# Kernel optimization log

Hardware: AMD Instinct MI355X
Metric: run time of the kernel (lower is better)

Reference implementation:

```python
import jax, jax.numpy as jnp
import numpy as np

FS = 16            # fixStride
LAST_RATIO = 0.5
TAUA, TAUB = 10.0, 0.1
TOT_EPOCHS = 100
EPS = 1e-20
SEED = 777


def _safe_norm(diff):
    # ||diff||_2 with subgradient 0 at 0 (matches torch.norm backward at 0)
    sq = jnp.sum(diff * diff, axis=-1)
    d = jnp.sqrt(jnp.where(sq > 0, sq, 1.0))
    return jnp.where(sq > 0, d, 0.0)


def _forward(x, w_score, b_score, att_params, num_graphs, epoch):
    BN, C = x.shape
    B = int(num_graphs)
    N = BN // B
    RES = N - FS + 1                       # rows per graph (unfold1d)
    MAXP = int(np.ceil(N * LAST_RATIO))    # max_pivot_count = ceil(N*last_ratio/init_ratio)

    # --- TopKPool scorer (init_ratio==1.0): permute nodes per graph by desc score
    scores = (x @ w_score + b_score) / jnp.sqrt(jnp.sum(w_score ** 2))
    perm = jnp.argsort(-scores.reshape(B, N), axis=-1, stable=True)      # [B,N]
    xg = jnp.take_along_axis(x.reshape(B, N, C), perm[..., None], axis=1)

    # --- sliding-window edges: row r -> dests r..r+FS-1, src node r
    dst = jnp.arange(RES)[:, None] + jnp.arange(FS)[None, :]             # [RES,FS]
    x_src = xg[:, :RES, :]                                               # [B,RES,C]
    x_dst = xg[:, dst, :]                                                # [B,RES,FS,C]

    # getSM_ei + scatter_softmax over rows: att = [x_s, x_d] @ att_params
    a1, a2 = att_params[:C], att_params[C:]
    sm = jax.nn.softmax((xg @ a1)[:, :RES, None] + (xg @ a2)[:, dst], axis=-1)  # [B,RES,FS]

    # getDM_ei (sigma=1): gaussian-kernel edge distances
    gk = jnp.exp(-_safe_norm(x_src[:, :, None, :] - x_dst) / 2.0) - EPS  # [B,RES,FS]

    # scatterSort: stable descending sort of gk per row
    order = jnp.argsort(-gk, axis=-1, stable=True)
    gk_sort = jnp.take_along_axis(gk, order, axis=-1)
    sm_sort = jnp.take_along_axis(sm, order, axis=-1)

    # per-rank column logits: scatter-sum of sorted attention over rows of each graph
    logits = jnp.broadcast_to(sm_sort.sum(axis=1)[:, None, :], (B, RES, FS))
    logits = logits.at[:, :, 0].set(-jnp.inf)            # mask rank-0 (self edge)

    # gumbel-softmax with annealed temperature
    tau0 = TAUA * (TAUB / TAUA) ** (float(epoch) / TOT_EPOCHS)
    g = jax.random.gumbel(jax.random.key(SEED), (B, RES, FS), jnp.float32)
    gmb = jax.nn.softmax((g + logits) / tau0, axis=-1)

    # per-row threshold and shifted distances (unsorted layout)
    ths = jnp.sum(gk_sort * gmb, axis=-1, keepdims=True)
    shifted = jax.nn.relu(gk - ths)                      # [B,RES,FS]

    # scatter_min over positions 1..FS-1 (position 0 excluded via index redirect)
    delta = (jnp.argmin(shifted[:, :, 1:], axis=-1) + 1).astype(jnp.int32)  # [B,RES]

    # innerLoopStar: follow skip pointers from row 0, up to MAXP pivots
    def chain(delta_g):
        def step(ptr, _):
            valid = ptr < RES
            piv = jnp.where(valid, ptr, -1)
            nxt = jnp.where(valid, ptr + delta_g[jnp.clip(ptr, 0, RES - 1)], jnp.int32(RES))
            return nxt, piv
        _, pivs = jax.lax.scan(step, jnp.int32(0), None, length=MAXP)
        return pivs

    pivots = jax.vmap(chain)(delta)                      # [B,MAXP], -1 padded
    mask = pivots >= 0
    pooled = jnp.take_along_axis(xg, jnp.clip(pivots, 0, N - 1)[..., None], axis=1)
    pooled = pooled * mask[..., None]                    # [B,MAXP,C]
    return pooled, shifted, pivots


def setup_inputs() -> dict:
    key = jax.random.key(0)
    k0, k1, k2, k3 = jax.random.split(key, 4)
    B, N, C = 128, 512, 64
    return {
        "x": jax.random.normal(k0, (B * N, C), jnp.float32),
        "w_score": jax.random.normal(k1, (C,), jnp.float32),
        "b_score": jax.random.normal(k2, (), jnp.float32),
        "att_params": jax.random.normal(k3, (2 * C,), jnp.float32),
        "num_graphs": B,
        "epoch": 10,
    }


def reference(x, w_score, b_score, att_params, num_graphs, epoch):
    return _forward(x, w_score, b_score, att_params, num_graphs, epoch)
```

## Files before the change

kernel.cpp:

```cpp
#include <hip/hip_runtime.h>
#include <math.h>

#define BB 128
#define NN 512
#define CC 64
#define FS 16
#define RES 497
#define MAXP 256
#define BN (BB*NN)
#define GT (BB*RES*FS)
#define WPB 16
#define NCH 32
#define ROWS (WPB+FS-1)
#define PITCH 66
#define TWPB 128
#define TCH 4

__device__ __forceinline__ unsigned rotl32(unsigned x, int d){ return (x<<d)|(x>>(32-d)); }

__device__ __forceinline__ void threefry777(unsigned x0, unsigned x1, unsigned &o0, unsigned &o1){
  const unsigned ks0 = 0u, ks1 = 777u;
  const unsigned ks2 = 0x1BD11BDAu ^ ks0 ^ ks1;
  x0 += ks0; x1 += ks1;
  x0+=x1; x1=rotl32(x1,13); x1^=x0;
  x0+=x1; x1=rotl32(x1,15); x1^=x0;
  x0+=x1; x1=rotl32(x1,26); x1^=x0;
  x0+=x1; x1=rotl32(x1, 6); x1^=x0;
  x0+=ks1; x1+=ks2+1u;
  x0+=x1; x1=rotl32(x1,17); x1^=x0;
  x0+=x1; x1=rotl32(x1,29); x1^=x0;
  x0+=x1; x1=rotl32(x1,16); x1^=x0;
  x0+=x1; x1=rotl32(x1,24); x1^=x0;
  x0+=ks2; x1+=ks0+2u;
  x0+=x1; x1=rotl32(x1,13); x1^=x0;
  x0+=x1; x1=rotl32(x1,15); x1^=x0;
  x0+=x1; x1=rotl32(x1,26); x1^=x0;
  x0+=x1; x1=rotl32(x1, 6); x1^=x0;
  x0+=ks0; x1+=ks1+3u;
  x0+=x1; x1=rotl32(x1,17); x1^=x0;
  x0+=x1; x1=rotl32(x1,29); x1^=x0;
  x0+=x1; x1=rotl32(x1,16); x1^=x0;
  x0+=x1; x1=rotl32(x1,24); x1^=x0;
  x0+=ks1; x1+=ks2+4u;
  x0+=x1; x1=rotl32(x1,13); x1^=x0;
  x0+=x1; x1=rotl32(x1,15); x1^=x0;
  x0+=x1; x1=rotl32(x1,26); x1^=x0;
  x0+=x1; x1=rotl32(x1, 6); x1^=x0;
  x0+=ks2; x1+=ks0+5u;
  o0 = x0; o1 = x1;
}

__device__ __forceinline__ float gumbel_at_f32(unsigned p){
  unsigned o0, o1;
  threefry777(0u, p, o0, o1);
  unsigned bits = o0 ^ o1;
  float fl = __uint_as_float((bits >> 9) | 0x3f800000u) - 1.0f;
  float u  = fmaxf(1.17549435e-38f, fl);
  return -logf(-logf(u));
}

__device__ __forceinline__ double wave_push_f64(double v, int dstLane){
  int lo = __double2loint(v), hi = __double2hiint(v);
  int plo = __builtin_amdgcn_ds_permute(dstLane<<2, lo);
  int phi = __builtin_amdgcn_ds_permute(dstLane<<2, hi);
  return __hiloint2double(phi, plo);
}

__global__ __launch_bounds__(NN) void k_scoresort(const float* __restrict__ x,
    const float* __restrict__ w, const float* __restrict__ bsc,
    const float* __restrict__ att, double* __restrict__ s1s,
    double* __restrict__ s2s, int* __restrict__ perm){
  int b = blockIdx.x, t = threadIdx.x;
  __shared__ double ss[NN];
  __shared__ int    si[NN];
  __shared__ double l1[NN], l2[NN];

  double wn=0.0, dw=0.0, d1=0.0, d2=0.0;
  #pragma unroll
  for (int c=0;c<CC;c++){ double wv=(double)w[c]; wn += wv*wv; }
  const float4* xr = (const float4*)(x + (size_t)(b*NN+t)*CC);
  #pragma unroll
  for (int q=0;q<CC/4;q++){
    float4 v = xr[q];
    double xv;
    xv=(double)v.x; dw+=xv*(double)w[4*q+0]; d1+=xv*(double)att[4*q+0]; d2+=xv*(double)att[CC+4*q+0];
    xv=(double)v.y; dw+=xv*(double)w[4*q+1]; d1+=xv*(double)att[4*q+1]; d2+=xv*(double)att[CC+4*q+1];
    xv=(double)v.z; dw+=xv*(double)w[4*q+2]; d1+=xv*(double)att[4*q+2]; d2+=xv*(double)att[CC+4*q+2];
    xv=(double)v.w; dw+=xv*(double)w[4*q+3]; d1+=xv*(double)att[4*q+3]; d2+=xv*(double)att[CC+4*q+3];
  }
  double s = (dw + (double)bsc[0]) / sqrt(wn);
  int idx = t;
  l1[t] = d1;
  l2[t] = d2;

  for (int k = 2; k <= NN; k <<= 1){
    bool up = ((t & k) == 0);
    for (int j = k >> 1; j >= 64; j >>= 1){
      ss[t] = s; si[t] = idx;
      __syncthreads();
      double os = ss[t ^ j]; int oi = si[t ^ j];
      bool first = ((t & j) == 0);
      bool cmp = (s > os) || (s == os && idx < oi);
      bool keep = (cmp == (first == up));
      if (!keep){ s = os; idx = oi; }
      __syncthreads();
    }
    #pragma unroll
    for (int j = 32; j > 0; j >>= 1){
      if (j <= (k >> 1)){
        double os = __shfl_xor(s, j, 64);
        int    oi = __shfl_xor(idx, j, 64);
        bool first = ((t & j) == 0);
        bool cmp = (s > os) || (s == os && idx < oi);
        bool keep = (cmp == (first == up));
        if (!keep){ s = os; idx = oi; }
      }
    }
  }
  __syncthreads();
  perm[b*NN + t] = idx;
  s1s[b*NN + t] = l1[idx];
  s2s[b*NN + t] = l2[idx];
}

__global__ __launch_bounds__(256) void k_passA(const float* __restrict__ x,
    const int* __restrict__ perm, const double* __restrict__ s1s,
    const double* __restrict__ s2s, double* __restrict__ gkd,
    unsigned char* __restrict__ rank8, double* __restrict__ partial){
  int b = blockIdx.y, ch = blockIdx.x, tid = threadIdx.x;
  int i0 = ch*WPB;
  int nwin  = min(WPB, RES - i0);
  int nrows = min(ROWS, NN - i0);
  __shared__ float  xs[ROWS*PITCH];
  __shared__ int    pg[ROWS];
  __shared__ double wred[4][FS];

  if (tid < nrows) pg[tid] = perm[b*NN + i0 + tid];
  __syncthreads();
  for (int u = tid; u < nrows*16; u += 256){
    int r = u >> 4, seg = u & 15;
    float4 v = ((const float4*)(x + (size_t)(b*NN + pg[r])*CC))[seg];
    float2* dst = (float2*)&xs[r*PITCH + seg*4];
    dst[0] = make_float2(v.x, v.y);
    dst[1] = make_float2(v.z, v.w);
  }
  __syncthreads();

  int w = tid >> 4, j = tid & 15;
  int lane = tid & 63, gbase = lane & 48, wv = tid >> 6;
  bool act = (w < nwin);
  int i = i0 + w;

  double sq = 0.0;
  const float* rs = &xs[w*PITCH];
  const float* rd = &xs[(w+j)*PITCH];
  #pragma unroll
  for (int c2=0;c2<CC/2;c2++){
    float2 a  = *(const float2*)&rs[2*c2];
    float2 bb = *(const float2*)&rd[2*c2];
    double d0 = (double)a.x - (double)bb.x;
    double d1v= (double)a.y - (double)bb.y;
    sq += d0*d0;
    sq += d1v*d1v;
  }
  double d   = (sq > 0.0) ? sqrt(sq) : 0.0;
  double gkv = exp(-d*0.5) - 1e-20;

  int drow = min(i + j, NN-1);
  double smt = s1s[b*NN + i] + s2s[b*NN + drow];
  double m = smt;
  #pragma unroll
  for (int off=8; off; off>>=1) m = fmax(m, __shfl_xor(m, off, 16));
  double em = exp(smt - m);
  double ssum = em;
  #pragma unroll
  for (int off=8; off; off>>=1) ssum += __shfl_xor(ssum, off, 16);
  double smn = em / ssum;

  int rank = 0;
  #pragma unroll
  for (int k=0;k<16;k++){
    double gkk = __shfl(gkv, gbase + k, 64);
    rank += ((gkk > gkv) || (gkk == gkv && k < j)) ? 1 : 0;
  }

  if (act){
    size_t base = ((size_t)b*RES + i)*FS;
    gkd[base + j]   = gkv;
    rank8[base + j] = (unsigned char)rank;
  }

  double contrib = act ? smn : 0.0;
  double srt = wave_push_f64(contrib, gbase + rank);
  srt += __shfl_xor(srt, 16, 64);
  srt += __shfl_xor(srt, 32, 64);
  if (lane < FS) wred[wv][lane] = srt;
  __syncthreads();
  if (tid < FS){
    partial[((size_t)b*NCH + ch)*FS + tid] =
        wred[0][tid] + wred[1][tid] + wred[2][tid] + wred[3][tid];
  }
}

__global__ __launch_bounds__(TWPB) void k_tail(const double* __restrict__ gkd,
    const unsigned char* __restrict__ rank8, const double* __restrict__ partial,
    const int* __restrict__ epoch_p, float* __restrict__ shifted_out,
    int* __restrict__ delta){
  int b = blockIdx.y, tid = threadIdx.x;
  int w0 = blockIdx.x*TWPB;
  int nw = min(TWPB, RES - w0);
  __shared__ double pl[NCH*FS];
  __shared__ double Ks[FS];
  __shared__ double gkL[TWPB*17];
  __shared__ double eL[TWPB*17];
  __shared__ uint4  rkL[TWPB];

  for (int u = tid; u < NCH*FS; u += TWPB) pl[u] = partial[(size_t)b*NCH*FS + u];
  {
    const double2* gsrc = (const double2*)(gkd + ((size_t)b*RES + w0)*FS);
    for (int u = tid; u < nw*8; u += TWPB){
      double2 v = gsrc[u];
      int row = u >> 3, col = (u & 7) << 1;
      gkL[row*17 + col]     = v.x;
      gkL[row*17 + col + 1] = v.y;
    }
  }
  if (tid < nw) rkL[tid] = ((const uint4*)rank8)[(size_t)b*RES + w0 + tid];
  __syncthreads();
  if (tid < FS){
    double a = 0.0;
    #pragma unroll
    for (int ch=0; ch<NCH; ch++) a += pl[ch*FS + tid];
    double tauB = 10.0 * exp(-4.605170185988091 * ((double)epoch_p[0] / 100.0));
    Ks[tid] = (tid == 0) ? 0.0 : exp(a / tauB);
  }
  __syncthreads();

  if (tid >= nw) return;
  int win = w0 + tid;
  size_t base = ((size_t)b*RES + win)*FS;
  double tau = 10.0 * exp(-4.605170185988091 * ((double)epoch_p[0] / 100.0));
  int gb = tid*17;

  eL[gb] = 0.0;
  double ssum = 0.0;
  for (int s=1;s<FS;s++){
    float g = gumbel_at_f32((unsigned)(base + (unsigned)s));
    double E = exp((double)g / tau) * Ks[s];
    eL[gb + s] = E;
    ssum += E;
  }

  uint4 rw = rkL[tid];
  unsigned rr[4] = { rw.x, rw.y, rw.z, rw.w };
  double ths = 0.0;
  #pragma unroll
  for (int j=0;j<FS;j++){
    int rk = (int)((rr[j>>2] >> ((j&3)*8)) & 15u);
    ths += gkL[gb + j] * (eL[gb + rk] / ssum);
  }

  double bv = 0.0; int bj = 1;
  #pragma unroll
  for (int q=0;q<4;q++){
    float4 sv;
    float* svp = (float*)&sv;
    #pragma unroll
    for (int r=0;r<4;r++){
      int j = q*4 + r;
      double shv = fmax(gkL[gb + j] - ths, 0.0);
      svp[r] = (float)shv;
      if (j == 1){ bv = shv; bj = 1; }
      else if (j > 1 && shv < bv){ bv = shv; bj = j; }
    }
    ((float4*)(shifted_out + base))[q] = sv;
  }
  delta[b*RES + win] = bj;
}

__global__ __launch_bounds__(256) void k_chainpool(const int* __restrict__ delta,
    const int* __restrict__ perm, const float* __restrict__ x,
    float* __restrict__ piv_out, float* __restrict__ pooled){
  int b = blockIdx.x, tid = threadIdx.x;
  __shared__ int tbl[8][512];
  __shared__ int pivS[MAXP];

  for (int i = tid; i < 512; i += 256){
    int v;
    if (i < RES){ v = i + delta[b*RES + i]; if (v > RES) v = RES; }
    else v = RES;
    tbl[0][i] = v;
  }
  __syncthreads();
  #pragma unroll
  for (int k=1;k<8;k++){
    int v0 = tbl[k-1][tid];
    int v1 = tbl[k-1][tid+256];
    tbl[k][tid]     = tbl[k-1][v0];
    tbl[k][tid+256] = tbl[k-1][v1];
    __syncthreads();
  }
  {
    int p = 0;
    #pragma unroll
    for (int k=0;k<8;k++) if ((tid>>k)&1) p = tbl[k][p];
    int piv = (p < RES) ? p : -1;
    pivS[tid] = piv;
    piv_out[b*MAXP + tid] = (float)piv;
  }
  __syncthreads();

  for (int u = tid; u < MAXP*16; u += 256){
    int bp = u >> 4, seg = u & 15;
    int piv = pivS[bp];
    float4 v = make_float4(0.f,0.f,0.f,0.f);
    if (piv >= 0){
      int src = perm[b*NN + piv];
      v = ((const float4*)(x + (size_t)(b*NN + src)*CC))[seg];
    }
    ((float4*)pooled)[(size_t)(b*MAXP + bp)*16 + seg] = v;
  }
}

extern "C" void kernel_launch(void* const* d_in, const int* in_sizes, int n_in,
                              void* d_out, int out_size, void* d_ws, size_t ws_size,
                              hipStream_t stream) {
  (void)in_sizes; (void)n_in; (void)out_size; (void)ws_size;
  const float* x    = (const float*)d_in[0];
  const float* w    = (const float*)d_in[1];
  const float* bsc  = (const float*)d_in[2];
  const float* att  = (const float*)d_in[3];
  const int*   epch = (const int*)d_in[5];

  double* s1s     = (double*)d_ws;
  double* s2s     = s1s + BN;
  double* gkd     = s2s + BN;
  double* partial = gkd + GT;
  int*    perm    = (int*)(partial + (size_t)BB*NCH*FS);
  int*    delta   = perm + BN;
  unsigned char* rank8 = (unsigned char*)(delta + BB*RES);

  float* out_pooled  = (float*)d_out;
  float* out_shifted = out_pooled + BB*MAXP*CC;
  float* out_piv     = out_shifted + (size_t)BB*RES*FS;

  k_scoresort<<<BB, NN, 0, stream>>>(x, w, bsc, att, s1s, s2s, perm);
  k_passA    <<<dim3(NCH, BB), 256, 0, stream>>>(x, perm, s1s, s2s, gkd, rank8, partial);
  k_tail     <<<dim3(TCH, BB), TWPB, 0, stream>>>(gkd, rank8, partial, epch, out_shifted, delta);
  k_chainpool<<<BB, 256, 0, stream>>>(delta, perm, x, out_piv, out_pooled);
}
```

Measured before the change: 70.18 us.

## Split each k_tail window across four lanes with shuffle reductions

The tail kernel now gives each sliding window to a group of four threads instead of one. Each lane computes four of the gumbel exponentials, loads four gk values and ranks directly from global memory, and writes one float4 of output. Partial sums, the threshold and the argmin are combined with wave shuffles. This raises parallelism (8x128 blocks of 256 threads) and shortens the serial per-thread gumbel and exp chains. In exchange it adds shuffle and synchronisation overhead and drops the shared-memory staging of gk.

```diff
diff --git a/kernel.cpp b/kernel.cpp
--- a/kernel.cpp
+++ b/kernel.cpp
@@ -13,8 +13,8 @@
 #define NCH 32
 #define ROWS (WPB+FS-1)
 #define PITCH 66
-#define TWPB 128
-#define TCH 4
+#define TW4 64
+#define TCH4 8
 
 __device__ __forceinline__ unsigned rotl32(unsigned x, int d){ return (x<<d)|(x>>(32-d)); }
 
@@ -202,80 +202,84 @@
   }
 }
 
-__global__ __launch_bounds__(TWPB) void k_tail(const double* __restrict__ gkd,
+__global__ __launch_bounds__(256) void k_tail(const double* __restrict__ gkd,
     const unsigned char* __restrict__ rank8, const double* __restrict__ partial,
     const int* __restrict__ epoch_p, float* __restrict__ shifted_out,
     int* __restrict__ delta){
   int b = blockIdx.y, tid = threadIdx.x;
-  int w0 = blockIdx.x*TWPB;
-  int nw = min(TWPB, RES - w0);
+  int grp = tid >> 2;
+  int L   = tid & 3;
+  int win = blockIdx.x*TW4 + grp;
   __shared__ double pl[NCH*FS];
   __shared__ double Ks[FS];
-  __shared__ double gkL[TWPB*17];
-  __shared__ double eL[TWPB*17];
-  __shared__ uint4  rkL[TWPB];
-
-  for (int u = tid; u < NCH*FS; u += TWPB) pl[u] = partial[(size_t)b*NCH*FS + u];
-  {
-    const double2* gsrc = (const double2*)(gkd + ((size_t)b*RES + w0)*FS);
-    for (int u = tid; u < nw*8; u += TWPB){
-      double2 v = gsrc[u];
-      int row = u >> 3, col = (u & 7) << 1;
-      gkL[row*17 + col]     = v.x;
-      gkL[row*17 + col + 1] = v.y;
-    }
-  }
-  if (tid < nw) rkL[tid] = ((const uint4*)rank8)[(size_t)b*RES + w0 + tid];
-  __syncthreads();
+  __shared__ double Es[TW4*17];
+
+  for (int u = tid; u < NCH*FS; u += 256) pl[u] = partial[(size_t)b*NCH*FS + u];
+  __syncthreads();
+  double tau = 10.0 * exp(-4.605170185988091 * ((double)epoch_p[0] / 100.0));
   if (tid < FS){
     double a = 0.0;
     #pragma unroll
     for (int ch=0; ch<NCH; ch++) a += pl[ch*FS + tid];
-    double tauB = 10.0 * exp(-4.605170185988091 * ((double)epoch_p[0] / 100.0));
-    Ks[tid] = (tid == 0) ? 0.0 : exp(a / tauB);
-  }
-  __syncthreads();
-
-  if (tid >= nw) return;
-  int win = w0 + tid;
-  size_t base = ((size_t)b*RES + win)*FS;
-  double tau = 10.0 * exp(-4.605170185988091 * ((double)epoch_p[0] / 100.0));
-  int gb = tid*17;
-
-  eL[gb] = 0.0;
+    Ks[tid] = (tid == 0) ? 0.0 : exp(a / tau);
+  }
+  __syncthreads();
+
+  bool act = (win < RES);
+  int winc = act ? win : (RES-1);
+  size_t base = ((size_t)b*RES + winc)*FS;
+  int eb = grp*17;
+
+  if (L == 3) Es[eb] = 0.0;
   double ssum = 0.0;
-  for (int s=1;s<FS;s++){
-    float g = gumbel_at_f32((unsigned)(base + (unsigned)s));
-    double E = exp((double)g / tau) * Ks[s];
-    eL[gb + s] = E;
-    ssum += E;
-  }
-
-  uint4 rw = rkL[tid];
-  unsigned rr[4] = { rw.x, rw.y, rw.z, rw.w };
+  #pragma unroll
+  for (int k=0;k<4;k++){
+    int s = L + 1 + 4*k;
+    if (s < FS){
+      float g = gumbel_at_f32((unsigned)(base + (unsigned)s));
+      double E = exp((double)g / tau) * Ks[s];
+      Es[eb + s] = E;
+      ssum += E;
+    }
+  }
+  ssum += __shfl_xor(ssum, 1, 64);
+  ssum += __shfl_xor(ssum, 2, 64);
+  __syncthreads();
+
+  double2 g01 = ((const double2*)(gkd + base))[2*L];
+  double2 g23 = ((const double2*)(gkd + base))[2*L + 1];
+  double gkv[4] = { g01.x, g01.y, g23.x, g23.y };
+  unsigned rw = ((const unsigned*)(rank8 + base))[L];
+
   double ths = 0.0;
   #pragma unroll
-  for (int j=0;j<FS;j++){
-    int rk = (int)((rr[j>>2] >> ((j&3)*8)) & 15u);
-    ths += gkL[gb + j] * (eL[gb + rk] / ssum);
-  }
-
-  double bv = 0.0; int bj = 1;
-  #pragma unroll
-  for (int q=0;q<4;q++){
-    float4 sv;
-    float* svp = (float*)&sv;
-    #pragma unroll
-    for (int r=0;r<4;r++){
-      int j = q*4 + r;
-      double shv = fmax(gkL[gb + j] - ths, 0.0);
-      svp[r] = (float)shv;
-      if (j == 1){ bv = shv; bj = 1; }
-      else if (j > 1 && shv < bv){ bv = shv; bj = j; }
-    }
-    ((float4*)(shifted_out + base))[q] = sv;
-  }
-  delta[b*RES + win] = bj;
+  for (int k=0;k<4;k++){
+    int rk = (int)((rw >> (k*8)) & 15u);
+    ths += gkv[k] * (Es[eb + rk] / ssum);
+  }
+  ths += __shfl_xor(ths, 1, 64);
+  ths += __shfl_xor(ths, 2, 64);
+
+  double bv = (double)INFINITY; int bj = 99;
+  float4 sv;
+  float* svp = (float*)&sv;
+  #pragma unroll
+  for (int k=0;k<4;k++){
+    int j = 4*L + k;
+    double shv = fmax(gkv[k] - ths, 0.0);
+    svp[k] = (float)shv;
+    if (j >= 1 && shv < bv){ bv = shv; bj = j; }
+  }
+  #pragma unroll
+  for (int off=1; off<=2; off<<=1){
+    double ov = __shfl_xor(bv, off, 64);
+    int    oi = __shfl_xor(bj, off, 64);
+    if (ov < bv || (ov == bv && oi < bj)){ bv = ov; bj = oi; }
+  }
+  if (act){
+    ((float4*)(shifted_out + base))[L] = sv;
+    if (L == 0) delta[b*RES + win] = bj;
+  }
 }
 
 __global__ __launch_bounds__(256) void k_chainpool(const int* __restrict__ delta,
@@ -346,6 +350,6 @@
 
   k_scoresort<<<BB, NN, 0, stream>>>(x, w, bsc, att, s1s, s2s, perm);
   k_passA    <<<dim3(NCH, BB), 256, 0, stream>>>(x, perm, s1s, s2s, gkd, rank8, partial);
-  k_tail     <<<dim3(TCH, BB), TWPB, 0, stream>>>(gkd, rank8, partial, epch, out_shifted, delta);
+  k_tail     <<<dim3(TCH4, BB), 256, 0, stream>>>(gkd, rank8, partial, epch, out_shifted, delta);
   k_chainpool<<<BB, 256, 0, stream>>>(delta, perm, x, out_piv, out_pooled);
 }
```

After: 62.80 us. 10.5% less time.
